# Kernel tuning notes

Hardware: AMD Instinct MI355X
Metric: run time of the kernel (lower is better)

## Reference

```python
import jax, jax.numpy as jnp
import numpy as np

B, T, S, D, H = 4, 1024, 1024, 1024, 16
DH = D // H  # head dim = 64
EPS = 1e-5
NEG = -1e9  # finite stand-in for -inf (grad-safe)


def setup_inputs() -> dict:
    key = jax.random.key(0)
    ks = jax.random.split(key, 9)
    std = D ** -0.5
    return {
        "q": jax.random.normal(ks[0], (B, T, D), jnp.float32),
        "k": jax.random.normal(ks[1], (B, S, D), jnp.float32),
        "v": jax.random.normal(ks[2], (B, S, D), jnp.float32),
        "attn_mask": jax.random.randint(ks[3], (T, S), 0, 2) == 1,
        "attn_bias": jax.random.normal(ks[4], (H, T, S), jnp.float32) * 0.1,
        "Wq": jax.random.normal(ks[5], (D, D), jnp.float32) * std,
        "Wk": jax.random.normal(ks[6], (D, D), jnp.float32) * std,
        "Wv": jax.random.normal(ks[7], (D, D), jnp.float32) * std,
        "Wo": jax.random.normal(ks[8], (D, D), jnp.float32) * std,
    }


def reference(q, k, v, attn_mask, attn_bias, Wq, Wk, Wv, Wo):
    # project and split heads: [B,T,D] -> [B,H,T,DH]
    qh = (q @ Wq.T).reshape(B, T, H, DH).transpose(0, 2, 1, 3) * (DH ** -0.5)
    kh = (k @ Wk.T).reshape(B, S, H, DH).transpose(0, 2, 1, 3)
    vh = (v @ Wv.T).reshape(B, S, H, DH).transpose(0, 2, 1, 3)
    # scores [B,H,T,S] with bias broadcast over batch, mask over (B,H)
    attn = jnp.einsum('bhtd,bhsd->bhts', qh, kh) + attn_bias
    attn = jnp.where(attn_mask, NEG, attn)
    # inverted softmax: normalize jointly over (heads, target) for each source pos
    a = jax.nn.softmax(attn.reshape(B, H * T, S), axis=1).reshape(B, H, T, S)
    a = jnp.where(attn_mask, 0.0, a)
    a = a / (a.sum(axis=-1, keepdims=True) + EPS)
    out = jnp.einsum('bhts,bhsd->bhtd', a, vh).transpose(0, 2, 1, 3).reshape(B, T, D)
    return out @ Wo.T
```

## Files before the change

kernel.cpp:

```cpp
#include <hip/hip_runtime.h>
#include <hip/hip_bf16.h>
#include <math.h>
#include <stdint.h>

#define B_ 4
#define T_ 1024
#define S_ 1024
#define D_ 1024
#define H_ 16
#define DH_ 64

static constexpr float EPSV = 1e-5f;
static constexpr float NEGV = -1e9f;

typedef __attribute__((ext_vector_type(8))) short short8;
typedef __attribute__((ext_vector_type(4))) float f32x4;

#define MFMA_BF16 __builtin_amdgcn_mfma_f32_16x16x32_bf16

__device__ __forceinline__ ushort f2bf(float f) {
  union { float f; unsigned u; } v; v.f = f;
  unsigned r = (v.u + 0x7FFFu + ((v.u >> 16) & 1u)) >> 16;
  return (ushort)r;
}
__device__ __forceinline__ float bf2f(ushort u) {
  union { unsigned u; float f; } v; v.u = (unsigned)u << 16;
  return v.f;
}

__device__ __forceinline__ void gl_lds16(const ushort* g, ushort* l) {
  __builtin_amdgcn_global_load_lds(
      (const __attribute__((address_space(1))) unsigned int*)g,
      (__attribute__((address_space(3))) unsigned int*)l, 16, 0, 0);
}

__global__ __launch_bounds__(256) void k_tobf16_3(const float* __restrict__ a,
                                                  const float* __restrict__ b,
                                                  const float* __restrict__ c,
                                                  ushort* __restrict__ oa,
                                                  ushort* __restrict__ ob,
                                                  ushort* __restrict__ oc) {
  const int which = blockIdx.x >> 12;
  const int local = blockIdx.x & 4095;
  const float* src = (which == 0) ? a : (which == 1) ? b : c;
  ushort* dst = (which == 0) ? oa : (which == 1) ? ob : oc;
  const int i = (local * 256 + threadIdx.x) * 4;
  float4 v = *(const float4*)(src + i);
  ushort4 o = make_ushort4(f2bf(v.x), f2bf(v.y), f2bf(v.z), f2bf(v.w));
  *(ushort4*)(dst + i) = o;
}

__global__ __launch_bounds__(256) void k_tobf16_w(const float* __restrict__ a,
                                                  const float* __restrict__ b,
                                                  const float* __restrict__ c,
                                                  const float* __restrict__ d,
                                                  ushort* __restrict__ oa,
                                                  ushort* __restrict__ ob,
                                                  ushort* __restrict__ oc,
                                                  ushort* __restrict__ od) {
  const int which = blockIdx.x >> 10;
  const int local = blockIdx.x & 1023;
  const float* src = (which == 0) ? a : (which == 1) ? b : (which == 2) ? c : d;
  ushort* dst = (which == 0) ? oa : (which == 1) ? ob : (which == 2) ? oc : od;
  const int i = (local * 256 + threadIdx.x) * 4;
  float4 v = *(const float4*)(src + i);
  ushort4 o = make_ushort4(f2bf(v.x), f2bf(v.y), f2bf(v.z), f2bf(v.w));
  *(ushort4*)(dst + i) = o;
}

__global__ __launch_bounds__(256) void k_fusebias(const float* __restrict__ bias,
                                                  const int* __restrict__ mask,
                                                  ushort* __restrict__ bm) {
  const size_t i = ((size_t)blockIdx.x * 256 + threadIdx.x) * 8;
  const size_t mi = i & (size_t)(T_ * S_ - 1);
  float4 b0 = *(const float4*)(bias + i);
  float4 b1 = *(const float4*)(bias + i + 4);
  int4 m0 = *(const int4*)(mask + mi);
  int4 m1 = *(const int4*)(mask + mi + 4);
  ushort o[8];
  o[0] = f2bf(m0.x ? NEGV : b0.x); o[1] = f2bf(m0.y ? NEGV : b0.y);
  o[2] = f2bf(m0.z ? NEGV : b0.z); o[3] = f2bf(m0.w ? NEGV : b0.w);
  o[4] = f2bf(m1.x ? NEGV : b1.x); o[5] = f2bf(m1.y ? NEGV : b1.y);
  o[6] = f2bf(m1.z ? NEGV : b1.z); o[7] = f2bf(m1.w ? NEGV : b1.w);
  *(uint4*)(bm + i) = *(uint4*)o;
}

template <int MODE>
__global__ __launch_bounds__(256) void k_gemm(const ushort* __restrict__ A,
                                              const ushort* __restrict__ W,
                                              void* __restrict__ Yv,
                                              float scale) {
  __shared__ ushort At[128][32];
  __shared__ ushort Wt[128][32];
  const int tid = threadIdx.x;
  const int l = tid & 63, w = tid >> 6;
  const int wm = (w >> 1) * 64, wn = (w & 1) * 64;
  const int r16 = l & 15, g = l >> 4;
  const int i0 = blockIdx.x * 128, j0 = blockIdx.y * 128;
  const int srow = (l >> 2), scol = (l & 3) << 3;
  f32x4 acc[4][4] = {};

  for (int k0 = 0; k0 < D_; k0 += 32) {
    __syncthreads();
#pragma unroll
    for (int u = 0; u < 2; ++u) {
      const int row = w * 32 + u * 16 + srow;
      gl_lds16(&A[(size_t)(i0 + row) * D_ + k0 + scol], &At[w * 32 + u * 16][0]);
      gl_lds16(&W[(size_t)(j0 + row) * D_ + k0 + scol], &Wt[w * 32 + u * 16][0]);
    }
    __syncthreads();
    short8 a0[4], b0[4];
#pragma unroll
    for (int i = 0; i < 4; ++i) a0[i] = *(const short8*)&At[wm + 16 * i + r16][g * 8];
#pragma unroll
    for (int j = 0; j < 4; ++j) b0[j] = *(const short8*)&Wt[wn + 16 * j + r16][g * 8];
#pragma unroll
    for (int i = 0; i < 4; ++i)
#pragma unroll
      for (int j = 0; j < 4; ++j)
        acc[i][j] = MFMA_BF16(a0[i], b0[j], acc[i][j], 0, 0, 0);
  }

#pragma unroll
  for (int i = 0; i < 4; ++i)
#pragma unroll
    for (int j = 0; j < 4; ++j)
#pragma unroll
      for (int r = 0; r < 4; ++r) {
        const int row = i0 + wm + 16 * i + 4 * g + r;
        const int col = j0 + wn + 16 * j + r16;
        const float v = acc[i][j][r] * scale;
        if (MODE == 0) {
          ((float*)Yv)[(size_t)row * D_ + col] = v;
        } else if (MODE == 1) {
          const int b = row >> 10, t = row & 1023;
          const int h = col >> 6, dh = col & 63;
          ((ushort*)Yv)[(((size_t)(b * H_ + h) * 1024) + t) * DH_ + dh] = f2bf(v);
        } else {
          const int b = row >> 10, s = row & 1023;
          const int h = col >> 6, dh = col & 63;
          ((ushort*)Yv)[((size_t)(b * H_ + h) * DH_ + dh) * 1024 + s] = f2bf(v);
        }
      }
}

__global__ __launch_bounds__(256, 4) void k_colstats(const ushort* __restrict__ Qh,
                                                     const ushort* __restrict__ Kh,
                                                     const ushort* __restrict__ biasm,
                                                     float* __restrict__ pc) {
  __shared__ ushort Qt[128][72];
  __shared__ ushort U[9216];
  ushort (*Kt)[72] = (ushort(*)[72])U;
  typedef ushort Row144[144];
  Row144* Bm0 = (Row144*)U;
  Row144* Bm1 = (Row144*)(U + 4608);

  const int z = blockIdx.z, b = z & 3, h = z >> 2;
  const int s0 = blockIdx.x * 128, t0 = blockIdx.y * 128;
  const int tid = threadIdx.x, l = tid & 63, w = tid >> 6;
  const int r16 = l & 15, g = l >> 4;

  const ushort* qsrc = Qh + ((size_t)((b * H_ + h) * 1024) + t0) * DH_;
  const ushort* ksrc = Kh + ((size_t)((b * H_ + h) * 1024) + s0) * DH_;
#pragma unroll
  for (int u = 0; u < 4; ++u) {
    const int lin = u * 256 + tid;
    const int row = lin >> 3, c8 = (lin & 7) << 3;
    *(uint4*)&Qt[row][c8] = *(const uint4*)&qsrc[(size_t)row * DH_ + c8];
    *(uint4*)&Kt[row][c8] = *(const uint4*)&ksrc[(size_t)row * DH_ + c8];
  }
  __syncthreads();

  f32x4 acc[8][2] = {};
#pragma unroll
  for (int kc = 0; kc < 2; ++kc) {
    short8 bk0 = *(const short8*)&Kt[w * 32 + r16][kc * 32 + g * 8];
    short8 bk1 = *(const short8*)&Kt[w * 32 + 16 + r16][kc * 32 + g * 8];
#pragma unroll
    for (int i = 0; i < 8; ++i) {
      short8 a = *(const short8*)&Qt[16 * i + r16][kc * 32 + g * 8];
      acc[i][0] = MFMA_BF16(a, bk0, acc[i][0], 0, 0, 0);
      acc[i][1] = MFMA_BF16(a, bk1, acc[i][1], 0, 0, 0);
    }
  }
  __syncthreads();

  const ushort* bsrc = biasm + ((size_t)h * 1024 + t0) * 1024 + s0;
#pragma unroll
  for (int u = 0; u < 2; ++u) {
    const int lin = u * 256 + tid;
    const int row = lin >> 4, c8 = (lin & 15) << 3;
    *(uint4*)&Bm0[row][c8] = *(const uint4*)&bsrc[(size_t)row * 1024 + c8];
  }
  __syncthreads();

  float cs0 = 0.f, cs1 = 0.f;
  const int col0 = w * 32 + r16;
#pragma unroll
  for (int c = 0; c < 4; ++c) {
    Row144* cur = (c & 1) ? Bm1 : Bm0;
    if (c < 3) {
      Row144* nxt = (c & 1) ? Bm0 : Bm1;
#pragma unroll
      for (int u = 0; u < 2; ++u) {
        const int lin = u * 256 + tid;
        const int row = lin >> 4, c8 = (lin & 15) << 3;
        *(uint4*)&nxt[row][c8] =
            *(const uint4*)&bsrc[(size_t)((c + 1) * 32 + row) * 1024 + c8];
      }
    }
#pragma unroll
    for (int ii = 0; ii < 2; ++ii) {
      const int i = 2 * c + ii;
      const int lrow = 16 * ii + 4 * g;
#pragma unroll
      for (int r = 0; r < 4; ++r) {
        cs0 += __expf(acc[i][0][r] + bf2f(cur[lrow + r][col0]));
        cs1 += __expf(acc[i][1][r] + bf2f(cur[lrow + r][col0 + 16]));
      }
    }
    __syncthreads();
  }

  cs0 += __shfl_xor(cs0, 16); cs0 += __shfl_xor(cs0, 32);
  cs1 += __shfl_xor(cs1, 16); cs1 += __shfl_xor(cs1, 32);
  if (g == 0) {
    const size_t base = ((size_t)b * 1024 + s0 + col0) * 128 + h * 8 + blockIdx.y;
    pc[base] = cs0;
    pc[base + 16 * 128] = cs1;
  }
}

__global__ __launch_bounds__(128) void k_combine(const float* __restrict__ pc,
                                                 float* __restrict__ Civ) {
  const int bs = blockIdx.x, tid = threadIdx.x;
  float c = pc[(size_t)bs * 128 + tid];
  __shared__ float sc[128];
  sc[tid] = c;
  __syncthreads();
  for (int off = 64; off > 0; off >>= 1) {
    if (tid < off) sc[tid] += sc[tid + off];
    __syncthreads();
  }
  if (tid == 0) {
    const float C = sc[0];
    Civ[bs] = (C > 0.f) ? 1.f / C : 0.f;
  }
}

__global__ __launch_bounds__(256, 3) void k_attn(const ushort* __restrict__ Qh,
                                                 const ushort* __restrict__ Kh,
                                                 const ushort* __restrict__ VhT,
                                                 const ushort* __restrict__ biasm,
                                                 const float* __restrict__ Civ,
                                                 ushort* __restrict__ O) {
  __shared__ ushort Kt[128][68];
  __shared__ ushort VtT[64][132];
  __shared__ ushort BmPt[64][132];
  __shared__ float Cih[128];
  __shared__ float Rp[4][64];

  const int bid = blockIdx.x;
  const int x8 = bid & 7;
  const int b = (bid >> 3) & 3;
  const int ht = (bid >> 5) * 8 + x8;
  const int h = ht >> 4, tt = ht & 15;
  const int t0 = tt * 64;
  const int bh = b * H_ + h;

  const int tid = threadIdx.x, l = tid & 63, w = tid >> 6;
  const int r16 = l & 15, g = l >> 4;
  const size_t kvbase = (size_t)bh * 1024 * DH_;
  const size_t vbase  = (size_t)bh * DH_ * 1024;

  short8 aq[4][2];
#pragma unroll
  for (int i = 0; i < 4; ++i) {
    const ushort* qr = Qh + ((size_t)bh * 1024 + t0 + 16 * i + r16) * DH_;
    aq[i][0] = *(const short8*)(qr + g * 8);
    aq[i][1] = *(const short8*)(qr + 32 + g * 8);
  }

  f32x4 aco[4] = {};
  float rloc[4] = {};

#pragma unroll 1
  for (int sc = 0; sc < 8; ++sc) {
    const int s0c = sc * 128;
    __syncthreads();

    {
      const ushort* ksrc = Kh + kvbase + (size_t)s0c * DH_;
#pragma unroll
      for (int u = 0; u < 4; ++u) {
        const int lin = u * 256 + tid;
        const int row = lin >> 3, c8 = (lin & 7) << 3;
        *(uint4*)&Kt[row][c8] = *(const uint4*)&ksrc[(size_t)row * DH_ + c8];
      }
      const ushort* vsrc = VhT + vbase + s0c;
      const ushort* bsrc = biasm + ((size_t)h * 1024 + t0) * 1024 + s0c;
#pragma unroll
      for (int u = 0; u < 4; ++u) {
        const int lin = u * 256 + tid;
        const int row = lin >> 4, c8 = (lin & 15) << 3;
        *(uint4*)&VtT[row][c8] = *(const uint4*)&vsrc[(size_t)row * 1024 + c8];
        *(uint4*)&BmPt[row][c8] = *(const uint4*)&bsrc[(size_t)row * 1024 + c8];
      }
      if (tid < 128) Cih[tid] = Civ[(size_t)b * 1024 + s0c + tid];
    }
    __syncthreads();

#pragma unroll
    for (int j2 = 0; j2 < 2; ++j2) {
      const int jf = 2 * w + j2;
      f32x4 as[4] = {};
      short8 kf0 = *(const short8*)&Kt[16 * jf + r16][g * 8];
      short8 kf1 = *(const short8*)&Kt[16 * jf + r16][32 + g * 8];
#pragma unroll
      for (int i = 0; i < 4; ++i) {
        as[i] = MFMA_BF16(kf0, aq[i][0], as[i], 0, 0, 0);
        as[i] = MFMA_BF16(kf1, aq[i][1], as[i], 0, 0, 0);
      }
      const int scol = 16 * jf + 4 * g;
      const float4 cv = *(const float4*)&Cih[scol];
#pragma unroll
      for (int i = 0; i < 4; ++i) {
        const int srow = 16 * i + r16;
        ushort4 bv4 = *(const ushort4*)&BmPt[srow][scol];
        ushort4 pw;
        float p;
        p = __expf(as[i][0] + bf2f(bv4.x)) * cv.x; rloc[i] += p; pw.x = f2bf(p);
        p = __expf(as[i][1] + bf2f(bv4.y)) * cv.y; rloc[i] += p; pw.y = f2bf(p);
        p = __expf(as[i][2] + bf2f(bv4.z)) * cv.z; rloc[i] += p; pw.z = f2bf(p);
        p = __expf(as[i][3] + bf2f(bv4.w)) * cv.w; rloc[i] += p; pw.w = f2bf(p);
        *(ushort4*)&BmPt[srow][scol] = pw;
      }
    }
    __syncthreads();

#pragma unroll
    for (int kc = 0; kc < 4; ++kc) {
      short8 ap = *(const short8*)&BmPt[16 * w + r16][kc * 32 + g * 8];
#pragma unroll
      for (int j = 0; j < 4; ++j) {
        short8 bv = *(const short8*)&VtT[16 * j + r16][kc * 32 + g * 8];
        aco[j] = MFMA_BF16(ap, bv, aco[j], 0, 0, 0);
      }
    }
  }

#pragma unroll
  for (int i = 0; i < 4; ++i) {
    float vsum = rloc[i];
    vsum += __shfl_xor(vsum, 16);
    vsum += __shfl_xor(vsum, 32);
    if (l < 16) Rp[w][16 * i + r16] = vsum;
  }
  __syncthreads();

#pragma unroll
  for (int j = 0; j < 4; ++j)
#pragma unroll
    for (int r = 0; r < 4; ++r) {
      const int tl = 16 * w + 4 * g + r;
      const float R = Rp[0][tl] + Rp[1][tl] + Rp[2][tl] + Rp[3][tl];
      const float o = aco[j][r] / (R + EPSV);
      const int d = 16 * j + r16;
      O[((size_t)(b * 1024) + t0 + tl) * D_ + h * DH_ + d] = f2bf(o);
    }
}

extern "C" void kernel_launch(void* const* d_in, const int* in_sizes, int n_in,
                              void* d_out, int out_size, void* d_ws, size_t ws_size,
                              hipStream_t stream) {
  (void)in_sizes; (void)n_in; (void)out_size; (void)ws_size;
  const float* q    = (const float*)d_in[0];
  const float* k    = (const float*)d_in[1];
  const float* v    = (const float*)d_in[2];
  const int*   mask = (const int*)d_in[3];
  const float* bias = (const float*)d_in[4];
  const float* Wq   = (const float*)d_in[5];
  const float* Wk   = (const float*)d_in[6];
  const float* Wv   = (const float*)d_in[7];
  const float* Wo   = (const float*)d_in[8];
  float* out = (float*)d_out;

  ushort* qb   = (ushort*)d_ws;
  ushort* kb   = qb + 4194304;
  ushort* vb   = kb + 4194304;
  ushort* Wqb  = vb + 4194304;
  ushort* Wkb  = Wqb + 1048576;
  ushort* Wvb  = Wkb + 1048576;
  ushort* Wob  = Wvb + 1048576;
  ushort* Qh   = Wob + 1048576;
  ushort* Kh   = Qh + 4194304;
  ushort* VhT  = Kh + 4194304;
  ushort* Ob   = VhT + 4194304;
  ushort* bm   = Ob + 4194304;
  float*  pc   = (float*)(bm + 16777216);
  float*  Civ  = pc + 524288;

  k_tobf16_3<<<12288, 256, 0, stream>>>(q, k, v, qb, kb, vb);
  k_tobf16_w<<<4096, 256, 0, stream>>>(Wq, Wk, Wv, Wo, Wqb, Wkb, Wvb, Wob);
  k_fusebias<<<8192, 256, 0, stream>>>(bias, mask, bm);

  k_gemm<1><<<dim3(32, 8), 256, 0, stream>>>(qb, Wqb, Qh, 0.125f);
  k_gemm<1><<<dim3(32, 8), 256, 0, stream>>>(kb, Wkb, Kh, 1.0f);
  k_gemm<2><<<dim3(32, 8), 256, 0, stream>>>(vb, Wvb, VhT, 1.0f);

  k_colstats<<<dim3(8, 8, 64), 256, 0, stream>>>(Qh, Kh, bm, pc);
  k_combine<<<4096, 128, 0, stream>>>(pc, Civ);
  k_attn<<<1024, 256, 0, stream>>>(Qh, Kh, VhT, bm, Civ, Ob);

  k_gemm<0><<<dim3(32, 8), 256, 0, stream>>>(Ob, Wob, out, 1.0f);
}
```

Measured before the change: 207.8 us.

## Merge prep kernels, fold log2e into scales, use exp2 and packed bf16 stores

Merges the three conversion and bias kernels into one launch. Pre-multiplies the Q scale and the bias by log2(e) so the exponentials become a single v_exp_f32 instruction. Packs the bf16 conversions with v_cvt_pk_bf16_f32 and vectorizes the transposed V store in the GEMM epilogue. These cut launch overhead and per-element ALU work in the softmax paths, at the cost of slightly different rounding in the bf16 bias and scores.

```diff
diff --git a/kernel.cpp b/kernel.cpp
--- a/kernel.cpp
+++ b/kernel.cpp
@@ -11,7 +11,9 @@
 #define DH_ 64
 
 static constexpr float EPSV = 1e-5f;
-static constexpr float NEGV = -1e9f;
+static constexpr float LOG2E = 1.4426950408889634f;
+static constexpr float NEG2 = -1.4426950e9f;
+static constexpr float SCALE_Q = 0.125f * LOG2E;
 
 typedef __attribute__((ext_vector_type(8))) short short8;
 typedef __attribute__((ext_vector_type(4))) float f32x4;
@@ -27,6 +29,16 @@
   union { unsigned u; float f; } v; v.u = (unsigned)u << 16;
   return v.f;
 }
+__device__ __forceinline__ float exp2_fast(float x) {
+  float r;
+  asm("v_exp_f32 %0, %1" : "=v"(r) : "v"(x));
+  return r;
+}
+__device__ __forceinline__ unsigned cvt_pk_bf16(float lo, float hi) {
+  unsigned r;
+  asm("v_cvt_pk_bf16_f32 %0, %1, %2" : "=v"(r) : "v"(lo), "v"(hi));
+  return r;
+}
 
 __device__ __forceinline__ void gl_lds16(const ushort* g, ushort* l) {
   __builtin_amdgcn_global_load_lds(
@@ -34,55 +46,46 @@
       (__attribute__((address_space(3))) unsigned int*)l, 16, 0, 0);
 }
 
-__global__ __launch_bounds__(256) void k_tobf16_3(const float* __restrict__ a,
-                                                  const float* __restrict__ b,
-                                                  const float* __restrict__ c,
-                                                  ushort* __restrict__ oa,
-                                                  ushort* __restrict__ ob,
-                                                  ushort* __restrict__ oc) {
-  const int which = blockIdx.x >> 12;
-  const int local = blockIdx.x & 4095;
-  const float* src = (which == 0) ? a : (which == 1) ? b : c;
-  ushort* dst = (which == 0) ? oa : (which == 1) ? ob : oc;
-  const int i = (local * 256 + threadIdx.x) * 4;
-  float4 v = *(const float4*)(src + i);
-  ushort4 o = make_ushort4(f2bf(v.x), f2bf(v.y), f2bf(v.z), f2bf(v.w));
-  *(ushort4*)(dst + i) = o;
-}
-
-__global__ __launch_bounds__(256) void k_tobf16_w(const float* __restrict__ a,
-                                                  const float* __restrict__ b,
-                                                  const float* __restrict__ c,
-                                                  const float* __restrict__ d,
-                                                  ushort* __restrict__ oa,
-                                                  ushort* __restrict__ ob,
-                                                  ushort* __restrict__ oc,
-                                                  ushort* __restrict__ od) {
-  const int which = blockIdx.x >> 10;
-  const int local = blockIdx.x & 1023;
-  const float* src = (which == 0) ? a : (which == 1) ? b : (which == 2) ? c : d;
-  ushort* dst = (which == 0) ? oa : (which == 1) ? ob : (which == 2) ? oc : od;
-  const int i = (local * 256 + threadIdx.x) * 4;
-  float4 v = *(const float4*)(src + i);
-  ushort4 o = make_ushort4(f2bf(v.x), f2bf(v.y), f2bf(v.z), f2bf(v.w));
-  *(ushort4*)(dst + i) = o;
-}
-
-__global__ __launch_bounds__(256) void k_fusebias(const float* __restrict__ bias,
-                                                  const int* __restrict__ mask,
-                                                  ushort* __restrict__ bm) {
-  const size_t i = ((size_t)blockIdx.x * 256 + threadIdx.x) * 8;
-  const size_t mi = i & (size_t)(T_ * S_ - 1);
-  float4 b0 = *(const float4*)(bias + i);
-  float4 b1 = *(const float4*)(bias + i + 4);
-  int4 m0 = *(const int4*)(mask + mi);
-  int4 m1 = *(const int4*)(mask + mi + 4);
-  ushort o[8];
-  o[0] = f2bf(m0.x ? NEGV : b0.x); o[1] = f2bf(m0.y ? NEGV : b0.y);
-  o[2] = f2bf(m0.z ? NEGV : b0.z); o[3] = f2bf(m0.w ? NEGV : b0.w);
-  o[4] = f2bf(m1.x ? NEGV : b1.x); o[5] = f2bf(m1.y ? NEGV : b1.y);
-  o[6] = f2bf(m1.z ? NEGV : b1.z); o[7] = f2bf(m1.w ? NEGV : b1.w);
-  *(uint4*)(bm + i) = *(uint4*)o;
+__global__ __launch_bounds__(256) void k_prep(
+    const float* __restrict__ q, const float* __restrict__ k,
+    const float* __restrict__ v, const float* __restrict__ Wq,
+    const float* __restrict__ Wk, const float* __restrict__ Wv,
+    const float* __restrict__ Wo, const float* __restrict__ bias,
+    const int* __restrict__ mask, ushort* __restrict__ qb,
+    ushort* __restrict__ kb, ushort* __restrict__ vb,
+    ushort* __restrict__ Wqb, ushort* __restrict__ Wkb,
+    ushort* __restrict__ Wvb, ushort* __restrict__ Wob,
+    ushort* __restrict__ bm) {
+  const int bid = blockIdx.x;
+  if (bid < 12288) {
+    const int which = bid >> 12, local = bid & 4095;
+    const float* src = (which == 0) ? q : (which == 1) ? k : v;
+    ushort* dst = (which == 0) ? qb : (which == 1) ? kb : vb;
+    const int i = (local * 256 + threadIdx.x) * 4;
+    float4 t = *(const float4*)(src + i);
+    *(ushort4*)(dst + i) = make_ushort4(f2bf(t.x), f2bf(t.y), f2bf(t.z), f2bf(t.w));
+  } else if (bid < 16384) {
+    const int wv_ = bid - 12288;
+    const int which = wv_ >> 10, local = wv_ & 1023;
+    const float* src = (which == 0) ? Wq : (which == 1) ? Wk : (which == 2) ? Wv : Wo;
+    ushort* dst = (which == 0) ? Wqb : (which == 1) ? Wkb : (which == 2) ? Wvb : Wob;
+    const int i = (local * 256 + threadIdx.x) * 4;
+    float4 t = *(const float4*)(src + i);
+    *(ushort4*)(dst + i) = make_ushort4(f2bf(t.x), f2bf(t.y), f2bf(t.z), f2bf(t.w));
+  } else {
+    const size_t i = ((size_t)(bid - 16384) * 256 + threadIdx.x) * 8;
+    const size_t mi = i & (size_t)(T_ * S_ - 1);
+    float4 b0 = *(const float4*)(bias + i);
+    float4 b1 = *(const float4*)(bias + i + 4);
+    int4 m0 = *(const int4*)(mask + mi);
+    int4 m1 = *(const int4*)(mask + mi + 4);
+    ushort o[8];
+    o[0] = f2bf(m0.x ? NEG2 : b0.x * LOG2E); o[1] = f2bf(m0.y ? NEG2 : b0.y * LOG2E);
+    o[2] = f2bf(m0.z ? NEG2 : b0.z * LOG2E); o[3] = f2bf(m0.w ? NEG2 : b0.w * LOG2E);
+    o[4] = f2bf(m1.x ? NEG2 : b1.x * LOG2E); o[5] = f2bf(m1.y ? NEG2 : b1.y * LOG2E);
+    o[6] = f2bf(m1.z ? NEG2 : b1.z * LOG2E); o[7] = f2bf(m1.w ? NEG2 : b1.w * LOG2E);
+    *(uint4*)(bm + i) = *(uint4*)o;
+  }
 }
 
 template <int MODE>
@@ -124,24 +127,32 @@
 #pragma unroll
   for (int i = 0; i < 4; ++i)
 #pragma unroll
-    for (int j = 0; j < 4; ++j)
-#pragma unroll
-      for (int r = 0; r < 4; ++r) {
-        const int row = i0 + wm + 16 * i + 4 * g + r;
+    for (int j = 0; j < 4; ++j) {
+      if (MODE == 2) {
+        const int row0 = i0 + wm + 16 * i + 4 * g;
         const int col = j0 + wn + 16 * j + r16;
-        const float v = acc[i][j][r] * scale;
-        if (MODE == 0) {
-          ((float*)Yv)[(size_t)row * D_ + col] = v;
-        } else if (MODE == 1) {
-          const int b = row >> 10, t = row & 1023;
-          const int h = col >> 6, dh = col & 63;
-          ((ushort*)Yv)[(((size_t)(b * H_ + h) * 1024) + t) * DH_ + dh] = f2bf(v);
-        } else {
-          const int b = row >> 10, s = row & 1023;
-          const int h = col >> 6, dh = col & 63;
-          ((ushort*)Yv)[((size_t)(b * H_ + h) * DH_ + dh) * 1024 + s] = f2bf(v);
+        const int bb = row0 >> 10, s = row0 & 1023;
+        const int hh = col >> 6, dh = col & 63;
+        ushort4 pw;
+        pw.x = f2bf(acc[i][j][0] * scale); pw.y = f2bf(acc[i][j][1] * scale);
+        pw.z = f2bf(acc[i][j][2] * scale); pw.w = f2bf(acc[i][j][3] * scale);
+        *(ushort4*)&((ushort*)Yv)[((size_t)(bb * H_ + hh) * DH_ + dh) * 1024 + s] = pw;
+      } else {
+#pragma unroll
+        for (int r = 0; r < 4; ++r) {
+          const int row = i0 + wm + 16 * i + 4 * g + r;
+          const int col = j0 + wn + 16 * j + r16;
+          const float vv = acc[i][j][r] * scale;
+          if (MODE == 0) {
+            ((float*)Yv)[(size_t)row * D_ + col] = vv;
+          } else {
+            const int b = row >> 10, t = row & 1023;
+            const int h = col >> 6, dh = col & 63;
+            ((ushort*)Yv)[(((size_t)(b * H_ + h) * 1024) + t) * DH_ + dh] = f2bf(vv);
+          }
         }
       }
+    }
 }
 
 __global__ __launch_bounds__(256, 4) void k_colstats(const ushort* __restrict__ Qh,
@@ -215,8 +226,8 @@
       const int lrow = 16 * ii + 4 * g;
 #pragma unroll
       for (int r = 0; r < 4; ++r) {
-        cs0 += __expf(acc[i][0][r] + bf2f(cur[lrow + r][col0]));
-        cs1 += __expf(acc[i][1][r] + bf2f(cur[lrow + r][col0 + 16]));
+        cs0 += exp2_fast(acc[i][0][r] + bf2f(cur[lrow + r][col0]));
+        cs1 += exp2_fast(acc[i][1][r] + bf2f(cur[lrow + r][col0 + 16]));
       }
     }
     __syncthreads();
@@ -327,13 +338,15 @@
       for (int i = 0; i < 4; ++i) {
         const int srow = 16 * i + r16;
         ushort4 bv4 = *(const ushort4*)&BmPt[srow][scol];
-        ushort4 pw;
-        float p;
-        p = __expf(as[i][0] + bf2f(bv4.x)) * cv.x; rloc[i] += p; pw.x = f2bf(p);
-        p = __expf(as[i][1] + bf2f(bv4.y)) * cv.y; rloc[i] += p; pw.y = f2bf(p);
-        p = __expf(as[i][2] + bf2f(bv4.z)) * cv.z; rloc[i] += p; pw.z = f2bf(p);
-        p = __expf(as[i][3] + bf2f(bv4.w)) * cv.w; rloc[i] += p; pw.w = f2bf(p);
-        *(ushort4*)&BmPt[srow][scol] = pw;
+        const float p0 = exp2_fast(as[i][0] + bf2f(bv4.x)) * cv.x;
+        const float p1 = exp2_fast(as[i][1] + bf2f(bv4.y)) * cv.y;
+        const float p2 = exp2_fast(as[i][2] + bf2f(bv4.z)) * cv.z;
+        const float p3 = exp2_fast(as[i][3] + bf2f(bv4.w)) * cv.w;
+        rloc[i] += (p0 + p1) + (p2 + p3);
+        uint2 pw;
+        pw.x = cvt_pk_bf16(p0, p1);
+        pw.y = cvt_pk_bf16(p2, p3);
+        *(uint2*)&BmPt[srow][scol] = pw;
       }
     }
     __syncthreads();
@@ -400,11 +413,10 @@
   float*  pc   = (float*)(bm + 16777216);
   float*  Civ  = pc + 524288;
 
-  k_tobf16_3<<<12288, 256, 0, stream>>>(q, k, v, qb, kb, vb);
-  k_tobf16_w<<<4096, 256, 0, stream>>>(Wq, Wk, Wv, Wo, Wqb, Wkb, Wvb, Wob);
-  k_fusebias<<<8192, 256, 0, stream>>>(bias, mask, bm);
-
-  k_gemm<1><<<dim3(32, 8), 256, 0, stream>>>(qb, Wqb, Qh, 0.125f);
+  k_prep<<<24576, 256, 0, stream>>>(q, k, v, Wq, Wk, Wv, Wo, bias, mask,
+                                    qb, kb, vb, Wqb, Wkb, Wvb, Wob, bm);
+
+  k_gemm<1><<<dim3(32, 8), 256, 0, stream>>>(qb, Wqb, Qh, SCALE_Q);
   k_gemm<1><<<dim3(32, 8), 256, 0, stream>>>(kb, Wkb, Kh, 1.0f);
   k_gemm<2><<<dim3(32, 8), 256, 0, stream>>>(vb, Wvb, VhT, 1.0f);
 
```

Result: faster. 196.1 us (-5.6%).
